# Optimization experiments

Measured on AMD Instinct MI355X. Metric: run time of the kernel, lower is better.

## Reference

```python
import jax, jax.numpy as jnp
import numpy as np

EPS = 1e-5  # torch BatchNorm2d default eps

def _bn(x, gamma, beta):
    # training-mode batch statistics over (N,H,W), per channel (biased variance)
    mean = jnp.mean(x, axis=(0, 2, 3), keepdims=True)
    var = jnp.var(x, axis=(0, 2, 3), keepdims=True)
    return gamma[None, :, None, None] * (x - mean) * jax.lax.rsqrt(var + EPS) + beta[None, :, None, None]

def _conv1x1(x, w, b):
    # (B,C,H,W) x (O,C) -> (B,O,H,W)
    return jnp.einsum('bchw,oc->bohw', x, w) + b[None, :, None, None]

def _maxpool2(x):
    B, C, H, W = x.shape
    return x.reshape(B, C, H // 2, 2, W // 2, 2).max(axis=(3, 5))

def setup_inputs() -> dict:
    key = jax.random.key(0)
    ks = jax.random.split(key, 5)
    B, C, H, W = 16, 256, 56, 56
    Ci, Cg = C // 8, C // 4
    def kaiming(k, o, i):
        return jax.random.normal(k, (o, i), jnp.float32) * np.float32(np.sqrt(2.0 / i))
    return {
        'x': jax.random.normal(ks[0], (B, C, H, W), jnp.float32),
        'bn1_gamma': jnp.ones((C,), jnp.float32),
        'bn1_beta': jnp.zeros((C,), jnp.float32),
        'w_g': kaiming(ks[1], Cg, C), 'b_g': jnp.zeros((Cg,), jnp.float32),
        'w_theta': kaiming(ks[2], Ci, C), 'b_theta': jnp.zeros((Ci,), jnp.float32),
        'w_phi': kaiming(ks[3], Ci, C), 'b_phi': jnp.zeros((Ci,), jnp.float32),
        'bn2_gamma': jnp.ones((Cg,), jnp.float32),
        'bn2_beta': jnp.zeros((Cg,), jnp.float32),
        'w_z': kaiming(ks[4], C, Cg), 'b_z': jnp.zeros((C,), jnp.float32),
    }

def reference(x, bn1_gamma, bn1_beta, w_g, b_g, w_theta, b_theta, w_phi, b_phi, bn2_gamma, bn2_beta, w_z, b_z):
    identity = x
    B, C, H, W = x.shape
    xa = jax.nn.relu(_bn(x, bn1_gamma, bn1_beta))
    g_x = _maxpool2(_conv1x1(xa, w_g, b_g))        # (B,Cg,H/2,W/2)
    phi_x = _maxpool2(_conv1x1(xa, w_phi, b_phi))  # (B,Ci,H/2,W/2)
    theta_x = _conv1x1(xa, w_theta, b_theta)       # (B,Ci,H,W)
    Cg = g_x.shape[1]
    Ci = theta_x.shape[1]
    Np = g_x.shape[2] * g_x.shape[3]               # subsampled positions (H/2*W/2)
    g_x = g_x.reshape(B, Cg, Np).transpose(0, 2, 1)      # (B,Np,Cg)
    phi_x = phi_x.reshape(B, Ci, Np)                     # (B,Ci,Np)
    theta_x = theta_x.reshape(B, Ci, H * W).transpose(0, 2, 1)  # (B,HW,Ci)
    f_div_C = jnp.einsum('bnc,bcm->bnm', theta_x, phi_x) / Np   # (B,HW,Np)
    y = jnp.einsum('bnm,bmc->bnc', f_div_C, g_x)                # (B,HW,Cg)
    y = y.transpose(0, 2, 1).reshape(B, Cg, H, W)
    w_y = _conv1x1(jax.nn.relu(_bn(y, bn2_gamma, bn2_beta)), w_z, b_z)
    return w_y + identity
```

## Files before the change

kernel.cpp:

```cpp
#include <hip/hip_runtime.h>
#include <hip/hip_bf16.h>

#define BB 16
#define CC 256
#define HWN 3136
#define NCG 64
#define NCI 32
#define NPP 784

typedef __attribute__((ext_vector_type(8))) short short8;
typedef __attribute__((ext_vector_type(4))) float floatx4;

__device__ __forceinline__ unsigned short f2bf(float f) {
    union { __hip_bfloat16 h; unsigned short u; } cv;
    cv.h = __float2bfloat16(f);
    return cv.u;
}
__device__ __forceinline__ float bf2f(unsigned short u) {
    return __uint_as_float(((unsigned)u) << 16);
}

__global__ __launch_bounds__(256) void k_head(const float* __restrict__ x,
                                              const float* __restrict__ w_t,
                                              const float* __restrict__ w_p,
                                              const float* __restrict__ w_g,
                                              const float* __restrict__ w_z,
                                              unsigned short* __restrict__ wcat,
                                              unsigned short* __restrict__ wzb,
                                              unsigned short* __restrict__ pool,
                                              float* __restrict__ zacc,
                                              float* __restrict__ bn1part) {
    int blk = blockIdx.x;
    int c = threadIdx.x;
    if (blk < 128) {
        int o = blk;
        const float* src = (o < 32) ? (w_t + o * CC)
                          : (o < 64) ? (w_p + (o - 32) * CC)
                                     : (w_g + (o - 64) * CC);
        wcat[o * CC + c] = f2bf(src[c]);
        {
            int r = o * 2 + (c >> 7);
            int kk = c & 127;
            if (kk < 72)
                wzb[r * 72 + kk] = (kk < 64) ? f2bf(w_z[r * 64 + kk]) : (unsigned short)0;
        }
        if (o < 96) {
            int b = c >> 4, kk = c & 15;
            pool[((size_t)(b * 96 + o)) * 800 + 784 + kk] = 0;
        }
        int idx = o * 256 + c;
        if (idx < 17024) zacc[idx] = 0.f;
        return;
    }
    int bc = blk - 128;
    const float4* p = (const float4*)(x + (size_t)bc * HWN);
    int tid = c;
    float s = 0.f, q = 0.f;
    for (int i = tid; i < 784; i += 256) {
        float4 v = p[i];
        s += v.x + v.y + v.z + v.w;
        q += v.x * v.x + v.y * v.y + v.z * v.z + v.w * v.w;
    }
    #pragma unroll
    for (int off = 32; off > 0; off >>= 1) {
        s += __shfl_down(s, off);
        q += __shfl_down(q, off);
    }
    __shared__ float sh[16];
    int wid = tid >> 6, lane = tid & 63;
    if (lane == 0) { sh[wid] = s; sh[8 + wid] = q; }
    __syncthreads();
    if (tid == 0) bn1part[bc]        = sh[0] + sh[1] + sh[2] + sh[3];
    if (tid == 1) bn1part[4096 + bc] = sh[8] + sh[9] + sh[10] + sh[11];
}

__global__ __launch_bounds__(256) void k_conv1(const float* __restrict__ x,
                                               const unsigned short* __restrict__ wcat,
                                               const float* __restrict__ bn1part,
                                               const float* __restrict__ gamma,
                                               const float* __restrict__ beta,
                                               const float* __restrict__ b_g,
                                               const float* __restrict__ b_t,
                                               const float* __restrict__ b_p,
                                               unsigned short* __restrict__ th,
                                               unsigned short* __restrict__ pool,
                                               float* __restrict__ T1g,
                                               float* __restrict__ Gg) {
    int b  = blockIdx.y;
    int bx = blockIdx.x;
    int hw0 = bx * 112;
    int tid = threadIdx.x;
    int wv = tid >> 6, ln = tid & 63;
    int col = ln & 15, quad = ln >> 4;

    __shared__ unsigned short smem[128 * 120];
    unsigned short* As = smem;
    unsigned short* Bs = smem + 4096;
    __shared__ float ab_s[512];
    __shared__ float bias_s[128];

    {
        const float inv = 1.0f / (BB * HWN);
        float s = 0.f, q = 0.f;
        #pragma unroll
        for (int b2 = 0; b2 < BB; ++b2) {
            s += bn1part[b2 * 256 + tid];
            q += bn1part[4096 + b2 * 256 + tid];
        }
        float mean = s * inv;
        float var  = q * inv - mean * mean;
        float a = gamma[tid] * rsqrtf(var + 1e-5f);
        ab_s[tid] = a;
        ab_s[CC + tid] = beta[tid] - mean * a;
    }
    if (tid < 128) {
        int o = tid;
        bias_s[o] = (o < 32) ? b_t[o] : (o < 64) ? b_p[o - 32] : b_g[o - 64];
    }
    __syncthreads();

    floatx4 acc[2][7];
    #pragma unroll
    for (int mt = 0; mt < 2; ++mt)
        for (int nt = 0; nt < 7; ++nt)
            acc[mt][nt] = (floatx4){0.f, 0.f, 0.f, 0.f};

    int p   = tid & 15;
    int hwq = tid >> 4;
    const float* xb = x + (size_t)(b * CC) * HWN + hw0;
    bool q1 = (hwq + 16) < 28;

    float4 pv0[2], pv1[2];
    {
        int c0 = 2 * p;
        pv0[0] = *(const float4*)(xb + (size_t)c0 * HWN + hwq * 4);
        pv1[0] = *(const float4*)(xb + (size_t)(c0 + 1) * HWN + hwq * 4);
        if (q1) {
            pv0[1] = *(const float4*)(xb + (size_t)c0 * HWN + (hwq + 16) * 4);
            pv1[1] = *(const float4*)(xb + (size_t)(c0 + 1) * HWN + (hwq + 16) * 4);
        }
    }

    for (int k0 = 0; k0 < CC; k0 += 32) {
        #pragma unroll
        for (int i = 0; i < 2; ++i) {
            int row = wv * 32 + i * 16 + (ln >> 2);
            int q   = ln & 3;
            const unsigned short* gp = wcat + row * CC + k0 + q * 8;
            __builtin_amdgcn_global_load_lds(
                (const __attribute__((address_space(1))) unsigned int*)gp,
                (__attribute__((address_space(3))) unsigned int*)&As[(wv * 2 + i) * 512],
                16, 0, 0);
        }
        {
            int c0 = k0 + 2 * p;
            float a0 = ab_s[c0],     d0 = ab_s[CC + c0];
            float a1 = ab_s[c0 + 1], d1 = ab_s[CC + c0 + 1];
            unsigned int* bw = (unsigned int*)Bs;
            #pragma unroll
            for (int t = 0; t < 2; ++t) {
                if (t == 0 || q1) {
                    int qi = hwq + 16 * t;
                    float4 v0 = pv0[t], v1 = pv1[t];
                    float r0[4] = { fmaxf(fmaf(a0, v0.x, d0), 0.f), fmaxf(fmaf(a0, v0.y, d0), 0.f),
                                    fmaxf(fmaf(a0, v0.z, d0), 0.f), fmaxf(fmaf(a0, v0.w, d0), 0.f) };
                    float r1[4] = { fmaxf(fmaf(a1, v1.x, d1), 0.f), fmaxf(fmaf(a1, v1.y, d1), 0.f),
                                    fmaxf(fmaf(a1, v1.z, d1), 0.f), fmaxf(fmaf(a1, v1.w, d1), 0.f) };
                    #pragma unroll
                    for (int i = 0; i < 4; ++i) {
                        unsigned int w = (unsigned int)f2bf(r0[i]) | ((unsigned int)f2bf(r1[i]) << 16);
                        bw[(qi * 4 + i) * 16 + p] = w;
                    }
                }
            }
        }
        __syncthreads();

        if (k0 + 32 < CC) {
            int c0 = k0 + 32 + 2 * p;
            pv0[0] = *(const float4*)(xb + (size_t)c0 * HWN + hwq * 4);
            pv1[0] = *(const float4*)(xb + (size_t)(c0 + 1) * HWN + hwq * 4);
            if (q1) {
                pv0[1] = *(const float4*)(xb + (size_t)c0 * HWN + (hwq + 16) * 4);
                pv1[1] = *(const float4*)(xb + (size_t)(c0 + 1) * HWN + (hwq + 16) * 4);
            }
        }

        short8 af0 = *(const short8*)&As[(wv * 32 +      col) * 32 + quad * 8];
        short8 af1 = *(const short8*)&As[(wv * 32 + 16 + col) * 32 + quad * 8];
        #pragma unroll
        for (int nt = 0; nt < 7; ++nt) {
            short8 bf = *(const short8*)&Bs[(nt * 16 + col) * 32 + quad * 8];
            acc[0][nt] = __builtin_amdgcn_mfma_f32_16x16x32_bf16(af0, bf, acc[0][nt], 0, 0, 0);
            acc[1][nt] = __builtin_amdgcn_mfma_f32_16x16x32_bf16(af1, bf, acc[1][nt], 0, 0, 0);
        }
        __syncthreads();
    }

    unsigned short* Ct = smem;
    #pragma unroll
    for (int mt = 0; mt < 2; ++mt) {
        int obase = wv * 32 + mt * 16 + quad * 4;
        #pragma unroll
        for (int r = 0; r < 4; ++r) {
            float bias = bias_s[obase + r];
            #pragma unroll
            for (int nt = 0; nt < 7; ++nt)
                Ct[(obase + r) * 120 + nt * 16 + col] = f2bf(acc[mt][nt][r] + bias);
        }
    }
    __syncthreads();

    #pragma unroll
    for (int i = 0; i < 4; ++i) {
        int e = tid + i * 256;
        if (e < 896) {
            int ch = e / 28, c4 = e - ch * 28;
            ushort4 v = *(const ushort4*)&Ct[ch * 120 + c4 * 4];
            *(ushort4*)&th[((size_t)(b * NCI + ch)) * HWN + hw0 + c4 * 4] = v;
        }
    }
    {
        int row = tid >> 3;
        int seg = tid & 7;
        float s = 0.f;
        #pragma unroll
        for (int j = 0; j < 14; ++j) s += bf2f(Ct[row * 120 + seg * 14 + j]);
        s += __shfl_down(s, 4);
        s += __shfl_down(s, 2);
        s += __shfl_down(s, 1);
        if (seg == 0) atomicAdd(&T1g[b * NCI + row], s);
    }
    {
        int m = wv >> 1, n = wv & 1;
        floatx4 g = (floatx4){0.f, 0.f, 0.f, 0.f};
        short8 z8 = (short8){0, 0, 0, 0, 0, 0, 0, 0};
        #pragma unroll
        for (int ks = 0; ks < 4; ++ks) {
            short8 ga, gb;
            if (ks < 3 || quad < 2) {
                ga = *(const short8*)&Ct[(m * 16 + col) * 120 + ks * 32 + quad * 8];
                gb = *(const short8*)&Ct[(n * 16 + col) * 120 + ks * 32 + quad * 8];
            } else {
                ga = z8; gb = z8;
            }
            g = __builtin_amdgcn_mfma_f32_16x16x32_bf16(ga, gb, g, 0, 0, 0);
        }
        float* gg = Gg + b * 1024 + (m * 16 + quad * 4) * 32 + n * 16 + col;
        #pragma unroll
        for (int r = 0; r < 4; ++r) atomicAdd(&gg[r * 32], g[r]);
    }
    #pragma unroll
    for (int i = 0; i < 11; ++i) {
        int e = tid + i * 256;
        if (e < 2688) {
            int ch = e / 28, m = e - ch * 28;
            const unsigned short* r0p = &Ct[(32 + ch) * 120 + 2 * m];
            float v = fmaxf(fmaxf(bf2f(r0p[0]), bf2f(r0p[1])),
                            fmaxf(bf2f(r0p[56]), bf2f(r0p[57])));
            pool[((size_t)(b * 96 + ch)) * 800 + bx * 28 + m] = f2bf(v);
        }
    }
}

__global__ __launch_bounds__(512) void k_sgemm(const unsigned short* __restrict__ pool,
                                               const float* __restrict__ T1g,
                                               const float* __restrict__ Gg,
                                               unsigned short* __restrict__ Sg,
                                               float* __restrict__ bn2acc) {
    int b = blockIdx.x;
    int tid = threadIdx.x;
    int wv = tid >> 6, ln = tid & 63;
    int col = ln & 15, quad = ln >> 4;
    __shared__ float Sred[8 * 2048];
    __shared__ float Gred[1024];
    __shared__ float T1s[32];
    __shared__ float shs[64], shq[64];

    if (tid < 64) { shs[tid] = 0.f; shq[tid] = 0.f; }
    if (tid < 32) T1s[tid] = T1g[b * NCI + tid];
    for (int idx = tid; idx < 1024; idx += 512) Gred[idx] = Gg[b * 1024 + idx];

    const unsigned short* gbase = pool + ((size_t)(b * 96 + 32)) * 800;
    const unsigned short* pbase = pool + ((size_t)(b * 96)) * 800;
    floatx4 acc[4][2];
    #pragma unroll
    for (int mt = 0; mt < 4; ++mt)
        for (int nt = 0; nt < 2; ++nt)
            acc[mt][nt] = (floatx4){0.f, 0.f, 0.f, 0.f};
    for (int s = wv; s < 25; s += 8) {
        int k0 = s * 32;
        short8 af[4], bfr[2];
        #pragma unroll
        for (int mt = 0; mt < 4; ++mt)
            af[mt] = *(const short8*)&gbase[(mt * 16 + col) * 800 + k0 + quad * 8];
        #pragma unroll
        for (int nt = 0; nt < 2; ++nt)
            bfr[nt] = *(const short8*)&pbase[(nt * 16 + col) * 800 + k0 + quad * 8];
        #pragma unroll
        for (int mt = 0; mt < 4; ++mt)
            #pragma unroll
            for (int nt = 0; nt < 2; ++nt)
                acc[mt][nt] = __builtin_amdgcn_mfma_f32_16x16x32_bf16(af[mt], bfr[nt], acc[mt][nt], 0, 0, 0);
    }
    #pragma unroll
    for (int mt = 0; mt < 4; ++mt)
        for (int nt = 0; nt < 2; ++nt)
            for (int r = 0; r < 4; ++r) {
                int cg = mt * 16 + quad * 4 + r;
                int ci = nt * 16 + col;
                Sred[wv * 2048 + cg * 32 + ci] = acc[mt][nt][r];
            }
    __syncthreads();

    for (int idx = tid; idx < 2048; idx += 512) {
        float s = 0.f;
        #pragma unroll
        for (int w = 0; w < 8; ++w) s += Sred[w * 2048 + idx];
        int cg = idx >> 5, ci = idx & 31;
        unsigned short h = f2bf(s * (1.0f / NPP));
        Sg[(size_t)b * 2560 + cg * 40 + ci] = h;
        Sred[idx] = bf2f(h);
    }
    __syncthreads();

    {
        int cg = tid & 63, part = tid >> 6;
        float sum = 0.f, sq = 0.f;
        #pragma unroll
        for (int i = 0; i < 4; ++i) {
            int ci = part * 4 + i;
            float sv = Sred[cg * 32 + ci];
            sum += sv * T1s[ci];
            float t = 0.f;
            #pragma unroll
            for (int cj = 0; cj < 32; ++cj)
                t += Gred[ci * 32 + cj] * Sred[cg * 32 + cj];
            sq += sv * t;
        }
        atomicAdd(&shs[cg], sum);
        atomicAdd(&shq[cg], sq);
    }
    __syncthreads();
    if (tid < 64) {
        atomicAdd(&bn2acc[tid], shs[tid]);
        atomicAdd(&bn2acc[64 + tid], shq[tid]);
    }
}

__global__ __launch_bounds__(256) void k_convz(const unsigned short* __restrict__ th,
                                               const unsigned short* __restrict__ Sg,
                                               const unsigned short* __restrict__ wzb,
                                               const float* __restrict__ bn2acc,
                                               const float* __restrict__ gamma,
                                               const float* __restrict__ beta,
                                               const float* __restrict__ b_z,
                                               const float* __restrict__ x,
                                               float* __restrict__ out) {
    int b = blockIdx.y;
    int hw0 = blockIdx.x * 64;
    int tid = threadIdx.x;
    int wv = tid >> 6, ln = tid & 63;
    int col = ln & 15, quad = ln >> 4;

    __shared__ unsigned short Wl[256 * 72];
    __shared__ unsigned short TS[5120];
    __shared__ float ab2_s[128];
    unsigned short* Tt = TS;
    unsigned short* St = TS + 2560;
    unsigned short* Yt = TS;

    for (int j = wv; j < 36; j += 4) {
        const unsigned short* gp = wzb + j * 512 + ln * 8;
        __builtin_amdgcn_global_load_lds(
            (const __attribute__((address_space(1))) unsigned int*)gp,
            (__attribute__((address_space(3))) unsigned int*)&Wl[j * 512],
            16, 0, 0);
    }
    if (tid < 64) {
        const float inv = 1.0f / (BB * HWN);
        float mean = bn2acc[tid] * inv;
        float var  = bn2acc[64 + tid] * inv - mean * mean;
        float a = gamma[tid] * rsqrtf(var + 1e-5f);
        ab2_s[tid] = a;
        ab2_s[64 + tid] = beta[tid] - mean * a;
    }
    {
        const unsigned int* sgw = (const unsigned int*)(Sg + (size_t)b * 2560);
        unsigned int* stw = (unsigned int*)St;
        for (int i = tid; i < 1280; i += 256) stw[i] = sgw[i];
    }
    {
        int p2 = tid & 15, hwq = tid >> 4;
        int c0 = 2 * p2;
        const unsigned short* tb = th + (size_t)(b * NCI) * HWN + hw0 + hwq * 4;
        ushort4 v0 = *(const ushort4*)(tb + (size_t)c0 * HWN);
        ushort4 v1 = *(const ushort4*)(tb + (size_t)(c0 + 1) * HWN);
        unsigned int* tw = (unsigned int*)Tt;
        tw[(hwq * 4 + 0) * 20 + p2] = (unsigned)v0.x | ((unsigned)v1.x << 16);
        tw[(hwq * 4 + 1) * 20 + p2] = (unsigned)v0.y | ((unsigned)v1.y << 16);
        tw[(hwq * 4 + 2) * 20 + p2] = (unsigned)v0.z | ((unsigned)v1.z << 16);
        tw[(hwq * 4 + 3) * 20 + p2] = (unsigned)v0.w | ((unsigned)v1.w << 16);
    }
    __syncthreads();

    short8 afy = *(const short8*)&Tt[(wv * 16 + col) * 40 + quad * 8];
    floatx4 yacc[4];
    #pragma unroll
    for (int nt = 0; nt < 4; ++nt) {
        short8 bf = *(const short8*)&St[(nt * 16 + col) * 40 + quad * 8];
        floatx4 z = (floatx4){0.f, 0.f, 0.f, 0.f};
        yacc[nt] = __builtin_amdgcn_mfma_f32_16x16x32_bf16(afy, bf, z, 0, 0, 0);
    }
    __syncthreads();

    #pragma unroll
    for (int nt = 0; nt < 4; ++nt) {
        int cg = nt * 16 + col;
        float a = ab2_s[cg], d = ab2_s[64 + cg];
        #pragma unroll
        for (int r = 0; r < 4; ++r) {
            int hwl = wv * 16 + quad * 4 + r;
            Yt[hwl * 72 + cg] = f2bf(fmaxf(fmaf(a, yacc[nt][r], d), 0.f));
        }
    }
    __syncthreads();

    floatx4 acc[16];
    #pragma unroll
    for (int nt = 0; nt < 16; ++nt) acc[nt] = (floatx4){0.f, 0.f, 0.f, 0.f};

    #pragma unroll
    for (int kk = 0; kk < 2; ++kk) {
        short8 afm = *(const short8*)&Yt[(wv * 16 + col) * 72 + kk * 32 + quad * 8];
        #pragma unroll
        for (int nt = 0; nt < 16; ++nt) {
            short8 bf = *(const short8*)&Wl[(nt * 16 + col) * 72 + kk * 32 + quad * 8];
            acc[nt] = __builtin_amdgcn_mfma_f32_16x16x32_bf16(afm, bf, acc[nt], 0, 0, 0);
        }
    }

    #pragma unroll
    for (int nt = 0; nt < 16; ++nt) {
        int co = nt * 16 + col;
        size_t base = ((size_t)(b * CC + co)) * HWN + hw0 + wv * 16 + quad * 4;
        float4 xv = *(const float4*)&x[base];
        float bz = b_z[co];
        float4 r = make_float4(acc[nt][0] + bz + xv.x, acc[nt][1] + bz + xv.y,
                               acc[nt][2] + bz + xv.z, acc[nt][3] + bz + xv.w);
        *(float4*)&out[base] = r;
    }
}

extern "C" void kernel_launch(void* const* d_in, const int* in_sizes, int n_in,
                              void* d_out, int out_size, void* d_ws, size_t ws_size,
                              hipStream_t stream) {
    (void)in_sizes; (void)n_in; (void)out_size; (void)ws_size;
    const float* x   = (const float*)d_in[0];
    const float* g1  = (const float*)d_in[1];
    const float* b1  = (const float*)d_in[2];
    const float* w_g = (const float*)d_in[3];
    const float* b_g = (const float*)d_in[4];
    const float* w_t = (const float*)d_in[5];
    const float* b_t = (const float*)d_in[6];
    const float* w_p = (const float*)d_in[7];
    const float* b_p = (const float*)d_in[8];
    const float* g2  = (const float*)d_in[9];
    const float* b2  = (const float*)d_in[10];
    const float* w_z = (const float*)d_in[11];
    const float* b_z = (const float*)d_in[12];
    float* out = (float*)d_out;

    float* ws      = (float*)d_ws;
    float* bn1part = ws;
    float* zacc    = ws + 8192;
    float* bn2acc  = ws + 8192;
    float* T1g     = ws + 8320;
    float* Gg      = ws + 8832;
    unsigned short* wcat = (unsigned short*)(ws + 25216);
    unsigned short* wzb  = (unsigned short*)(ws + 41600);
    unsigned short* th   = (unsigned short*)(ws + 50816);
    unsigned short* pool = (unsigned short*)(ws + 853632);
    unsigned short* Sg   = (unsigned short*)(ws + 1468032);

    k_head  <<<dim3(4224),     dim3(256), 0, stream>>>(x, w_t, w_p, w_g, w_z, wcat, wzb, pool, zacc, bn1part);
    k_conv1 <<<dim3(28, BB),   dim3(256), 0, stream>>>(x, wcat, bn1part, g1, b1, b_g, b_t, b_p, th, pool, T1g, Gg);
    k_sgemm <<<dim3(BB),       dim3(512), 0, stream>>>(pool, T1g, Gg, Sg, bn2acc);
    k_convz <<<dim3(49, BB),   dim3(256), 0, stream>>>(th, Sg, wzb, bn2acc, g2, b2, b_z, x, out);
}
```

Baseline: 170.5 us.

## Fuse four stage kernels into one cooperative persistent kernel with grid syncs

Replaces the four separate launches (head/BN1 stats, conv1, S-gemm, convz) with a single cooperative kernel of 256 persistent blocks that loops over tiles and separates stages with grid-wide syncs. It also prefetches the convz weights and the first theta tile before the last grid sync. The goal is to remove launch gaps and tail effects between stages. In exchange, conv1 runs on 256 blocks for 448 tiles, giving about two waves with uneven load. The S-gemm stage uses only 16 blocks while the rest wait, and each grid sync adds cost. The old path is kept as a fallback if the cooperative launch fails.

```diff
diff --git a/kernel.cpp b/kernel.cpp
--- a/kernel.cpp
+++ b/kernel.cpp
@@ -1,12 +1,15 @@
 #include <hip/hip_runtime.h>
 #include <hip/hip_bf16.h>
+#include <hip/hip_cooperative_groups.h>
+
+namespace cg = cooperative_groups;
 
 #define BB 16
 #define CC 256
 #define HWN 3136
-#define NCG 64
 #define NCI 32
 #define NPP 784
+#define GRID 256
 
 typedef __attribute__((ext_vector_type(8))) short short8;
 typedef __attribute__((ext_vector_type(4))) float floatx4;
@@ -20,16 +23,432 @@
     return __uint_as_float(((unsigned)u) << 16);
 }
 
-__global__ __launch_bounds__(256) void k_head(const float* __restrict__ x,
-                                              const float* __restrict__ w_t,
-                                              const float* __restrict__ w_p,
-                                              const float* __restrict__ w_g,
-                                              const float* __restrict__ w_z,
-                                              unsigned short* __restrict__ wcat,
-                                              unsigned short* __restrict__ wzb,
-                                              unsigned short* __restrict__ pool,
-                                              float* __restrict__ zacc,
-                                              float* __restrict__ bn1part) {
+__device__ __forceinline__ void stage_Tt(unsigned short* Tt, const unsigned short* th,
+                                         int b, int hw0, int tid) {
+    int p2 = tid & 15, hwq = tid >> 4;
+    int c0 = 2 * p2;
+    const unsigned short* tb = th + (size_t)(b * NCI) * HWN + hw0 + hwq * 4;
+    ushort4 v0 = *(const ushort4*)(tb + (size_t)c0 * HWN);
+    ushort4 v1 = *(const ushort4*)(tb + (size_t)(c0 + 1) * HWN);
+    unsigned int* tw = (unsigned int*)Tt;
+    tw[(hwq * 4 + 0) * 20 + p2] = (unsigned)v0.x | ((unsigned)v1.x << 16);
+    tw[(hwq * 4 + 1) * 20 + p2] = (unsigned)v0.y | ((unsigned)v1.y << 16);
+    tw[(hwq * 4 + 2) * 20 + p2] = (unsigned)v0.z | ((unsigned)v1.z << 16);
+    tw[(hwq * 4 + 3) * 20 + p2] = (unsigned)v0.w | ((unsigned)v1.w << 16);
+}
+
+__global__ __launch_bounds__(256, 1) void k_fused(
+    const float* __restrict__ x,
+    const float* __restrict__ bn1g, const float* __restrict__ bn1b,
+    const float* __restrict__ w_g, const float* __restrict__ b_g,
+    const float* __restrict__ w_t, const float* __restrict__ b_t,
+    const float* __restrict__ w_p, const float* __restrict__ b_p,
+    const float* __restrict__ bn2g, const float* __restrict__ bn2b,
+    const float* __restrict__ w_z, const float* __restrict__ b_z,
+    float* __restrict__ out,
+    unsigned short* __restrict__ wcat, unsigned short* __restrict__ wzb,
+    unsigned short* __restrict__ th, unsigned short* __restrict__ pool,
+    unsigned short* __restrict__ Sg,
+    float* __restrict__ bn1part, float* __restrict__ zacc,
+    float* __restrict__ bn2acc, float* __restrict__ T1g, float* __restrict__ Gg)
+{
+    cg::grid_group gr = cg::this_grid();
+    int blk = blockIdx.x;
+    int tid = threadIdx.x;
+    int wv = tid >> 6, ln = tid & 63;
+    int col = ln & 15, quad = ln >> 4;
+
+    __shared__ unsigned short regA[18432];
+    __shared__ unsigned short TSm[5120];
+    __shared__ float abm[512];
+    __shared__ float bias_s[128];
+
+    if (blk < 128) {
+        int o = blk, c = tid;
+        const float* src = (o < 32) ? (w_t + o * CC)
+                          : (o < 64) ? (w_p + (o - 32) * CC)
+                                     : (w_g + (o - 64) * CC);
+        wcat[o * CC + c] = f2bf(src[c]);
+        int r = o * 2 + (c >> 7), kk = c & 127;
+        if (kk < 72)
+            wzb[r * 72 + kk] = (kk < 64) ? f2bf(w_z[r * 64 + kk]) : (unsigned short)0;
+    }
+    for (int i = blk * 256 + tid; i < 17024; i += GRID * 256) zacc[i] = 0.f;
+    for (int i = blk * 256 + tid; i < 24576; i += GRID * 256) {
+        int o = i >> 8, b = (i >> 4) & 15, kk = i & 15;
+        pool[((size_t)(b * 96 + o)) * 800 + 784 + kk] = 0;
+    }
+    {
+        int gw = blk * 4 + wv;
+        for (int p = gw; p < 4096; p += 4 * GRID) {
+            const float4* pp = (const float4*)(x + (size_t)p * HWN);
+            float s = 0.f, q = 0.f;
+            for (int i = ln; i < 784; i += 64) {
+                float4 v = pp[i];
+                s += v.x + v.y + v.z + v.w;
+                q += v.x * v.x + v.y * v.y + v.z * v.z + v.w * v.w;
+            }
+            #pragma unroll
+            for (int off = 32; off > 0; off >>= 1) {
+                s += __shfl_down(s, off);
+                q += __shfl_down(q, off);
+            }
+            if (ln == 0) { bn1part[p] = s; bn1part[4096 + p] = q; }
+        }
+    }
+    __threadfence();
+    gr.sync();
+    __threadfence();
+
+    {
+        unsigned short* As = regA;
+        unsigned short* Bs = regA + 4096;
+        float* ab_s = abm;
+
+        {
+            const float inv = 1.0f / (BB * HWN);
+            float s = 0.f, q = 0.f;
+            #pragma unroll
+            for (int b2 = 0; b2 < BB; ++b2) {
+                s += bn1part[b2 * 256 + tid];
+                q += bn1part[4096 + b2 * 256 + tid];
+            }
+            float mean = s * inv;
+            float var  = q * inv - mean * mean;
+            float a = bn1g[tid] * rsqrtf(var + 1e-5f);
+            ab_s[tid] = a;
+            ab_s[CC + tid] = bn1b[tid] - mean * a;
+        }
+        if (tid < 128) {
+            int o = tid;
+            bias_s[o] = (o < 32) ? b_t[o] : (o < 64) ? b_p[o - 32] : b_g[o - 64];
+        }
+        __syncthreads();
+
+        for (int t = blk; t < 448; t += GRID) {
+            int b  = t / 28;
+            int bx = t % 28;
+            int hw0 = bx * 112;
+
+            floatx4 acc[2][7];
+            #pragma unroll
+            for (int mt = 0; mt < 2; ++mt)
+                for (int nt = 0; nt < 7; ++nt)
+                    acc[mt][nt] = (floatx4){0.f, 0.f, 0.f, 0.f};
+
+            int p   = tid & 15;
+            int hwq = tid >> 4;
+            const float* xb = x + (size_t)(b * CC) * HWN + hw0;
+            bool q1 = (hwq + 16) < 28;
+
+            float4 pv0[2], pv1[2];
+            {
+                int c0 = 2 * p;
+                pv0[0] = *(const float4*)(xb + (size_t)c0 * HWN + hwq * 4);
+                pv1[0] = *(const float4*)(xb + (size_t)(c0 + 1) * HWN + hwq * 4);
+                if (q1) {
+                    pv0[1] = *(const float4*)(xb + (size_t)c0 * HWN + (hwq + 16) * 4);
+                    pv1[1] = *(const float4*)(xb + (size_t)(c0 + 1) * HWN + (hwq + 16) * 4);
+                }
+            }
+
+            for (int k0 = 0; k0 < CC; k0 += 32) {
+                #pragma unroll
+                for (int i = 0; i < 2; ++i) {
+                    int row = wv * 32 + i * 16 + (ln >> 2);
+                    int q   = ln & 3;
+                    const unsigned short* gp = wcat + row * CC + k0 + q * 8;
+                    __builtin_amdgcn_global_load_lds(
+                        (const __attribute__((address_space(1))) unsigned int*)gp,
+                        (__attribute__((address_space(3))) unsigned int*)&As[(wv * 2 + i) * 512],
+                        16, 0, 0);
+                }
+                {
+                    int c0 = k0 + 2 * p;
+                    float a0 = ab_s[c0],     d0 = ab_s[CC + c0];
+                    float a1 = ab_s[c0 + 1], d1 = ab_s[CC + c0 + 1];
+                    unsigned int* bw = (unsigned int*)Bs;
+                    #pragma unroll
+                    for (int tt = 0; tt < 2; ++tt) {
+                        if (tt == 0 || q1) {
+                            int qi = hwq + 16 * tt;
+                            float4 v0 = pv0[tt], v1 = pv1[tt];
+                            float r0[4] = { fmaxf(fmaf(a0, v0.x, d0), 0.f), fmaxf(fmaf(a0, v0.y, d0), 0.f),
+                                            fmaxf(fmaf(a0, v0.z, d0), 0.f), fmaxf(fmaf(a0, v0.w, d0), 0.f) };
+                            float r1[4] = { fmaxf(fmaf(a1, v1.x, d1), 0.f), fmaxf(fmaf(a1, v1.y, d1), 0.f),
+                                            fmaxf(fmaf(a1, v1.z, d1), 0.f), fmaxf(fmaf(a1, v1.w, d1), 0.f) };
+                            #pragma unroll
+                            for (int i = 0; i < 4; ++i) {
+                                unsigned int w = (unsigned int)f2bf(r0[i]) | ((unsigned int)f2bf(r1[i]) << 16);
+                                bw[(qi * 4 + i) * 16 + p] = w;
+                            }
+                        }
+                    }
+                }
+                __syncthreads();
+
+                if (k0 + 32 < CC) {
+                    int c0 = k0 + 32 + 2 * p;
+                    pv0[0] = *(const float4*)(xb + (size_t)c0 * HWN + hwq * 4);
+                    pv1[0] = *(const float4*)(xb + (size_t)(c0 + 1) * HWN + hwq * 4);
+                    if (q1) {
+                        pv0[1] = *(const float4*)(xb + (size_t)c0 * HWN + (hwq + 16) * 4);
+                        pv1[1] = *(const float4*)(xb + (size_t)(c0 + 1) * HWN + (hwq + 16) * 4);
+                    }
+                }
+
+                short8 af0 = *(const short8*)&As[(wv * 32 +      col) * 32 + quad * 8];
+                short8 af1 = *(const short8*)&As[(wv * 32 + 16 + col) * 32 + quad * 8];
+                #pragma unroll
+                for (int nt = 0; nt < 7; ++nt) {
+                    short8 bf = *(const short8*)&Bs[(nt * 16 + col) * 32 + quad * 8];
+                    acc[0][nt] = __builtin_amdgcn_mfma_f32_16x16x32_bf16(af0, bf, acc[0][nt], 0, 0, 0);
+                    acc[1][nt] = __builtin_amdgcn_mfma_f32_16x16x32_bf16(af1, bf, acc[1][nt], 0, 0, 0);
+                }
+                __syncthreads();
+            }
+
+            unsigned short* Ct = regA;
+            #pragma unroll
+            for (int mt = 0; mt < 2; ++mt) {
+                int obase = wv * 32 + mt * 16 + quad * 4;
+                #pragma unroll
+                for (int r = 0; r < 4; ++r) {
+                    float bias = bias_s[obase + r];
+                    #pragma unroll
+                    for (int nt = 0; nt < 7; ++nt)
+                        Ct[(obase + r) * 120 + nt * 16 + col] = f2bf(acc[mt][nt][r] + bias);
+                }
+            }
+            __syncthreads();
+
+            #pragma unroll
+            for (int i = 0; i < 4; ++i) {
+                int e = tid + i * 256;
+                if (e < 896) {
+                    int ch = e / 28, c4 = e - ch * 28;
+                    ushort4 v = *(const ushort4*)&Ct[ch * 120 + c4 * 4];
+                    *(ushort4*)&th[((size_t)(b * NCI + ch)) * HWN + hw0 + c4 * 4] = v;
+                }
+            }
+            {
+                int row = tid >> 3, seg = tid & 7;
+                float s = 0.f;
+                #pragma unroll
+                for (int j = 0; j < 14; ++j) s += bf2f(Ct[row * 120 + seg * 14 + j]);
+                s += __shfl_down(s, 4);
+                s += __shfl_down(s, 2);
+                s += __shfl_down(s, 1);
+                if (seg == 0) atomicAdd(&T1g[b * NCI + row], s);
+            }
+            {
+                int m = wv >> 1, n = wv & 1;
+                floatx4 g = (floatx4){0.f, 0.f, 0.f, 0.f};
+                short8 z8 = (short8){0, 0, 0, 0, 0, 0, 0, 0};
+                #pragma unroll
+                for (int ks = 0; ks < 4; ++ks) {
+                    short8 ga, gb;
+                    if (ks < 3 || quad < 2) {
+                        ga = *(const short8*)&Ct[(m * 16 + col) * 120 + ks * 32 + quad * 8];
+                        gb = *(const short8*)&Ct[(n * 16 + col) * 120 + ks * 32 + quad * 8];
+                    } else {
+                        ga = z8; gb = z8;
+                    }
+                    g = __builtin_amdgcn_mfma_f32_16x16x32_bf16(ga, gb, g, 0, 0, 0);
+                }
+                float* ggp = Gg + b * 1024 + (m * 16 + quad * 4) * 32 + n * 16 + col;
+                #pragma unroll
+                for (int r = 0; r < 4; ++r) atomicAdd(&ggp[r * 32], g[r]);
+            }
+            #pragma unroll
+            for (int i = 0; i < 11; ++i) {
+                int e = tid + i * 256;
+                if (e < 2688) {
+                    int ch = e / 28, m = e - ch * 28;
+                    const unsigned short* r0p = &Ct[(32 + ch) * 120 + 2 * m];
+                    float v = fmaxf(fmaxf(bf2f(r0p[0]), bf2f(r0p[1])),
+                                    fmaxf(bf2f(r0p[56]), bf2f(r0p[57])));
+                    pool[((size_t)(b * 96 + ch)) * 800 + bx * 28 + m] = f2bf(v);
+                }
+            }
+            __syncthreads();
+        }
+    }
+    __threadfence();
+    gr.sync();
+    __threadfence();
+
+    if (blk < 16) {
+        int b = blk;
+        float* Sred = (float*)regA;
+        float* Gred = (float*)TSm;
+        float* T1s  = abm;
+        float* shs  = abm + 64;
+        float* shq  = abm + 128;
+        if (tid < 64) { shs[tid] = 0.f; shq[tid] = 0.f; }
+        if (tid < 32) T1s[tid] = T1g[b * NCI + tid];
+        for (int idx = tid; idx < 1024; idx += 256) Gred[idx] = Gg[b * 1024 + idx];
+
+        const unsigned short* gbase = pool + ((size_t)(b * 96 + 32)) * 800;
+        const unsigned short* pbase = pool + ((size_t)(b * 96)) * 800;
+        floatx4 acc[4][2];
+        #pragma unroll
+        for (int mt = 0; mt < 4; ++mt)
+            for (int nt = 0; nt < 2; ++nt)
+                acc[mt][nt] = (floatx4){0.f, 0.f, 0.f, 0.f};
+        for (int ks = wv; ks < 25; ks += 4) {
+            int k0 = ks * 32;
+            short8 af[4], bfr[2];
+            #pragma unroll
+            for (int mt = 0; mt < 4; ++mt)
+                af[mt] = *(const short8*)&gbase[(mt * 16 + col) * 800 + k0 + quad * 8];
+            #pragma unroll
+            for (int nt = 0; nt < 2; ++nt)
+                bfr[nt] = *(const short8*)&pbase[(nt * 16 + col) * 800 + k0 + quad * 8];
+            #pragma unroll
+            for (int mt = 0; mt < 4; ++mt)
+                #pragma unroll
+                for (int nt = 0; nt < 2; ++nt)
+                    acc[mt][nt] = __builtin_amdgcn_mfma_f32_16x16x32_bf16(af[mt], bfr[nt], acc[mt][nt], 0, 0, 0);
+        }
+        #pragma unroll
+        for (int mt = 0; mt < 4; ++mt)
+            for (int nt = 0; nt < 2; ++nt)
+                for (int r = 0; r < 4; ++r)
+                    Sred[wv * 2048 + (mt * 16 + quad * 4 + r) * 32 + nt * 16 + col] = acc[mt][nt][r];
+        __syncthreads();
+
+        for (int idx = tid; idx < 2048; idx += 256) {
+            float s = Sred[idx] + Sred[2048 + idx] + Sred[4096 + idx] + Sred[6144 + idx];
+            int cgi = idx >> 5, ci = idx & 31;
+            unsigned short h = f2bf(s * (1.0f / NPP));
+            Sg[(size_t)b * 2560 + cgi * 40 + ci] = h;
+            Sred[idx] = bf2f(h);
+        }
+        __syncthreads();
+
+        {
+            int cgi = tid & 63, part = tid >> 6;
+            float sum = 0.f, sq = 0.f;
+            #pragma unroll
+            for (int i = 0; i < 8; ++i) {
+                int ci = part * 8 + i;
+                float sv = Sred[cgi * 32 + ci];
+                sum += sv * T1s[ci];
+                float t2 = 0.f;
+                #pragma unroll
+                for (int cj = 0; cj < 32; ++cj)
+                    t2 += Gred[ci * 32 + cj] * Sred[cgi * 32 + cj];
+                sq += sv * t2;
+            }
+            atomicAdd(&shs[cgi], sum);
+            atomicAdd(&shq[cgi], sq);
+        }
+        __syncthreads();
+        if (tid < 64) {
+            atomicAdd(&bn2acc[tid], shs[tid]);
+            atomicAdd(&bn2acc[64 + tid], shq[tid]);
+        }
+        __syncthreads();
+    }
+    for (int j = wv; j < 36; j += 4) {
+        const unsigned short* gp = wzb + j * 512 + ln * 8;
+        __builtin_amdgcn_global_load_lds(
+            (const __attribute__((address_space(1))) unsigned int*)gp,
+            (__attribute__((address_space(3))) unsigned int*)&regA[j * 512],
+            16, 0, 0);
+    }
+    stage_Tt(TSm, th, blk / 49, (blk % 49) * 64, tid);
+    __threadfence();
+    gr.sync();
+    __threadfence();
+
+    {
+        unsigned short* Wl = regA;
+        unsigned short* Tt = TSm;
+        unsigned short* St = TSm + 2560;
+        unsigned short* Yt = TSm;
+
+        if (tid < 64) {
+            const float inv = 1.0f / (BB * HWN);
+            float mean = bn2acc[tid] * inv;
+            float var  = bn2acc[64 + tid] * inv - mean * mean;
+            float a = bn2g[tid] * rsqrtf(var + 1e-5f);
+            abm[tid] = a;
+            abm[64 + tid] = bn2b[tid] - mean * a;
+        }
+
+        for (int t = blk; t < 784; t += GRID) {
+            int b = t / 49, hw0 = (t % 49) * 64;
+            if (t != blk) {
+                __syncthreads();
+                stage_Tt(Tt, th, b, hw0, tid);
+            }
+            {
+                const unsigned int* sgw = (const unsigned int*)(Sg + (size_t)b * 2560);
+                unsigned int* stw = (unsigned int*)St;
+                for (int i = tid; i < 1280; i += 256) stw[i] = sgw[i];
+            }
+            __syncthreads();
+
+            short8 afy = *(const short8*)&Tt[(wv * 16 + col) * 40 + quad * 8];
+            floatx4 yacc[4];
+            #pragma unroll
+            for (int nt = 0; nt < 4; ++nt) {
+                short8 bf = *(const short8*)&St[(nt * 16 + col) * 40 + quad * 8];
+                floatx4 z = (floatx4){0.f, 0.f, 0.f, 0.f};
+                yacc[nt] = __builtin_amdgcn_mfma_f32_16x16x32_bf16(afy, bf, z, 0, 0, 0);
+            }
+            __syncthreads();
+
+            #pragma unroll
+            for (int nt = 0; nt < 4; ++nt) {
+                int cgi = nt * 16 + col;
+                float a = abm[cgi], d = abm[64 + cgi];
+                #pragma unroll
+                for (int r = 0; r < 4; ++r) {
+                    int hwl = wv * 16 + quad * 4 + r;
+                    Yt[hwl * 72 + cgi] = f2bf(fmaxf(fmaf(a, yacc[nt][r], d), 0.f));
+                }
+            }
+            __syncthreads();
+
+            floatx4 acc[16];
+            #pragma unroll
+            for (int nt = 0; nt < 16; ++nt) acc[nt] = (floatx4){0.f, 0.f, 0.f, 0.f};
+            #pragma unroll
+            for (int kk = 0; kk < 2; ++kk) {
+                short8 afm = *(const short8*)&Yt[(wv * 16 + col) * 72 + kk * 32 + quad * 8];
+                #pragma unroll
+                for (int nt = 0; nt < 16; ++nt) {
+                    short8 bf = *(const short8*)&Wl[(nt * 16 + col) * 72 + kk * 32 + quad * 8];
+                    acc[nt] = __builtin_amdgcn_mfma_f32_16x16x32_bf16(afm, bf, acc[nt], 0, 0, 0);
+                }
+            }
+            #pragma unroll
+            for (int nt = 0; nt < 16; ++nt) {
+                int co = nt * 16 + col;
+                size_t base = ((size_t)(b * CC + co)) * HWN + hw0 + wv * 16 + quad * 4;
+                float4 xv = *(const float4*)&x[base];
+                float bz = b_z[co];
+                float4 r = make_float4(acc[nt][0] + bz + xv.x, acc[nt][1] + bz + xv.y,
+                                       acc[nt][2] + bz + xv.z, acc[nt][3] + bz + xv.w);
+                *(float4*)&out[base] = r;
+            }
+        }
+    }
+}
+
+__global__ __launch_bounds__(256) void kf_head(const float* __restrict__ x,
+                                               const float* __restrict__ w_t,
+                                               const float* __restrict__ w_p,
+                                               const float* __restrict__ w_g,
+                                               const float* __restrict__ w_z,
+                                               unsigned short* __restrict__ wcat,
+                                               unsigned short* __restrict__ wzb,
+                                               unsigned short* __restrict__ pool,
+                                               float* __restrict__ zacc,
+                                               float* __restrict__ bn1part) {
     int blk = blockIdx.x;
     int c = threadIdx.x;
     if (blk < 128) {
@@ -74,18 +493,18 @@
     if (tid == 1) bn1part[4096 + bc] = sh[8] + sh[9] + sh[10] + sh[11];
 }
 
-__global__ __launch_bounds__(256) void k_conv1(const float* __restrict__ x,
-                                               const unsigned short* __restrict__ wcat,
-                                               const float* __restrict__ bn1part,
-                                               const float* __restrict__ gamma,
-                                               const float* __restrict__ beta,
-                                               const float* __restrict__ b_g,
-                                               const float* __restrict__ b_t,
-                                               const float* __restrict__ b_p,
-                                               unsigned short* __restrict__ th,
-                                               unsigned short* __restrict__ pool,
-                                               float* __restrict__ T1g,
-                                               float* __restrict__ Gg) {
+__global__ __launch_bounds__(256) void kf_conv1(const float* __restrict__ x,
+                                                const unsigned short* __restrict__ wcat,
+                                                const float* __restrict__ bn1part,
+                                                const float* __restrict__ gamma,
+                                                const float* __restrict__ beta,
+                                                const float* __restrict__ b_g,
+                                                const float* __restrict__ b_t,
+                                                const float* __restrict__ b_p,
+                                                unsigned short* __restrict__ th,
+                                                unsigned short* __restrict__ pool,
+                                                float* __restrict__ T1g,
+                                                float* __restrict__ Gg) {
     int b  = blockIdx.y;
     int bx = blockIdx.x;
     int hw0 = bx * 112;
@@ -221,8 +640,7 @@
         }
     }
     {
-        int row = tid >> 3;
-        int seg = tid & 7;
+        int row = tid >> 3, seg = tid & 7;
         float s = 0.f;
         #pragma unroll
         for (int j = 0; j < 14; ++j) s += bf2f(Ct[row * 120 + seg * 14 + j]);
@@ -246,9 +664,9 @@
             }
             g = __builtin_amdgcn_mfma_f32_16x16x32_bf16(ga, gb, g, 0, 0, 0);
         }
-        float* gg = Gg + b * 1024 + (m * 16 + quad * 4) * 32 + n * 16 + col;
-        #pragma unroll
-        for (int r = 0; r < 4; ++r) atomicAdd(&gg[r * 32], g[r]);
+        float* ggp = Gg + b * 1024 + (m * 16 + quad * 4) * 32 + n * 16 + col;
+        #pragma unroll
+        for (int r = 0; r < 4; ++r) atomicAdd(&ggp[r * 32], g[r]);
     }
     #pragma unroll
     for (int i = 0; i < 11; ++i) {
@@ -263,11 +681,11 @@
     }
 }
 
-__global__ __launch_bounds__(512) void k_sgemm(const unsigned short* __restrict__ pool,
-                                               const float* __restrict__ T1g,
-                                               const float* __restrict__ Gg,
-                                               unsigned short* __restrict__ Sg,
-                                               float* __restrict__ bn2acc) {
+__global__ __launch_bounds__(512) void kf_sgemm(const unsigned short* __restrict__ pool,
+                                                const float* __restrict__ T1g,
+                                                const float* __restrict__ Gg,
+                                                unsigned short* __restrict__ Sg,
+                                                float* __restrict__ bn2acc) {
     int b = blockIdx.x;
     int tid = threadIdx.x;
     int wv = tid >> 6, ln = tid & 63;
@@ -306,11 +724,8 @@
     #pragma unroll
     for (int mt = 0; mt < 4; ++mt)
         for (int nt = 0; nt < 2; ++nt)
-            for (int r = 0; r < 4; ++r) {
-                int cg = mt * 16 + quad * 4 + r;
-                int ci = nt * 16 + col;
-                Sred[wv * 2048 + cg * 32 + ci] = acc[mt][nt][r];
-            }
+            for (int r = 0; r < 4; ++r)
+                Sred[wv * 2048 + (mt * 16 + quad * 4 + r) * 32 + nt * 16 + col] = acc[mt][nt][r];
     __syncthreads();
 
     for (int idx = tid; idx < 2048; idx += 512) {
@@ -348,15 +763,15 @@
     }
 }
 
-__global__ __launch_bounds__(256) void k_convz(const unsigned short* __restrict__ th,
-                                               const unsigned short* __restrict__ Sg,
-                                               const unsigned short* __restrict__ wzb,
-                                               const float* __restrict__ bn2acc,
-                                               const float* __restrict__ gamma,
-                                               const float* __restrict__ beta,
-                                               const float* __restrict__ b_z,
-                                               const float* __restrict__ x,
-                                               float* __restrict__ out) {
+__global__ __launch_bounds__(256) void kf_convz(const unsigned short* __restrict__ th,
+                                                const unsigned short* __restrict__ Sg,
+                                                const unsigned short* __restrict__ wzb,
+                                                const float* __restrict__ bn2acc,
+                                                const float* __restrict__ gamma,
+                                                const float* __restrict__ beta,
+                                                const float* __restrict__ b_z,
+                                                const float* __restrict__ x,
+                                                float* __restrict__ out) {
     int b = blockIdx.y;
     int hw0 = blockIdx.x * 64;
     int tid = threadIdx.x;
@@ -390,18 +805,7 @@
         unsigned int* stw = (unsigned int*)St;
         for (int i = tid; i < 1280; i += 256) stw[i] = sgw[i];
     }
-    {
-        int p2 = tid & 15, hwq = tid >> 4;
-        int c0 = 2 * p2;
-        const unsigned short* tb = th + (size_t)(b * NCI) * HWN + hw0 + hwq * 4;
-        ushort4 v0 = *(const ushort4*)(tb + (size_t)c0 * HWN);
-        ushort4 v1 = *(const ushort4*)(tb + (size_t)(c0 + 1) * HWN);
-        unsigned int* tw = (unsigned int*)Tt;
-        tw[(hwq * 4 + 0) * 20 + p2] = (unsigned)v0.x | ((unsigned)v1.x << 16);
-        tw[(hwq * 4 + 1) * 20 + p2] = (unsigned)v0.y | ((unsigned)v1.y << 16);
-        tw[(hwq * 4 + 2) * 20 + p2] = (unsigned)v0.z | ((unsigned)v1.z << 16);
-        tw[(hwq * 4 + 3) * 20 + p2] = (unsigned)v0.w | ((unsigned)v1.w << 16);
-    }
+    stage_Tt(Tt, th, b, hw0, tid);
     __syncthreads();
 
     short8 afy = *(const short8*)&Tt[(wv * 16 + col) * 40 + quad * 8];
@@ -483,8 +887,14 @@
     unsigned short* pool = (unsigned short*)(ws + 853632);
     unsigned short* Sg   = (unsigned short*)(ws + 1468032);
 
-    k_head  <<<dim3(4224),     dim3(256), 0, stream>>>(x, w_t, w_p, w_g, w_z, wcat, wzb, pool, zacc, bn1part);
-    k_conv1 <<<dim3(28, BB),   dim3(256), 0, stream>>>(x, wcat, bn1part, g1, b1, b_g, b_t, b_p, th, pool, T1g, Gg);
-    k_sgemm <<<dim3(BB),       dim3(512), 0, stream>>>(pool, T1g, Gg, Sg, bn2acc);
-    k_convz <<<dim3(49, BB),   dim3(256), 0, stream>>>(th, Sg, wzb, bn2acc, g2, b2, b_z, x, out);
+    void* args[] = { &x, &g1, &b1, &w_g, &b_g, &w_t, &b_t, &w_p, &b_p, &g2, &b2, &w_z, &b_z,
+                     &out, &wcat, &wzb, &th, &pool, &Sg, &bn1part, &zacc, &bn2acc, &T1g, &Gg };
+    hipError_t err = hipLaunchCooperativeKernel((void*)k_fused, dim3(GRID), dim3(256),
+                                                args, 0u, stream);
+    if (err != hipSuccess) {
+        kf_head  <<<dim3(4224),    dim3(256), 0, stream>>>(x, w_t, w_p, w_g, w_z, wcat, wzb, pool, zacc, bn1part);
+        kf_conv1 <<<dim3(28, BB),  dim3(256), 0, stream>>>(x, wcat, bn1part, g1, b1, b_g, b_t, b_p, th, pool, T1g, Gg);
+        kf_sgemm <<<dim3(BB),      dim3(512), 0, stream>>>(pool, T1g, Gg, Sg, bn2acc);
+        kf_convz <<<dim3(49, BB),  dim3(256), 0, stream>>>(th, Sg, wzb, bn2acc, g2, b2, b_z, x, out);
+    }
 }
```

Measured after the change: 416.2 us. 2.44x slower.
